# Performance work log

Hardware: AMD Instinct MI355X
Metric: run time of the kernel (lower is better)

The kernel has to match this reference:

```python
import jax, jax.numpy as jnp
import numpy as np

H, C = 5, 128          # heads, hidden_channels
NUM_GRAPHS = 500
N_NODES, N_EDGES = 20000, 320000


def gat_layer(x, edge_attr, src, dst, W, We, a_src, a_dst, a_edge, b):
    """PyG GATConv with edge_dim, add_self_loops=True, fill_value='mean', concat heads."""
    N = x.shape[0]
    ed = edge_attr.dtype
    # self-loop edge_attr = scatter-mean of incoming edge_attr per target node
    deg = jax.ops.segment_sum(jnp.ones((dst.shape[0],), ed), dst, num_segments=N)
    loop_attr = jax.ops.segment_sum(edge_attr, dst, num_segments=N) / jnp.maximum(deg, 1.0)[:, None]
    loop = jnp.arange(N, dtype=src.dtype)
    s = jnp.concatenate([src, loop])
    d = jnp.concatenate([dst, loop])
    ea = jnp.concatenate([edge_attr, loop_attr], axis=0)
    h = (x @ W).reshape(N, H, C)            # [N,H,C]
    e = (ea @ We).reshape(-1, H, C)         # [E2,H,C]
    a_l = (h * a_src).sum(-1)               # [N,H]
    a_r = (h * a_dst).sum(-1)               # [N,H]
    a_e = (e * a_edge).sum(-1)              # [E2,H]
    alpha = jax.nn.leaky_relu(a_l[s] + a_r[d] + a_e, 0.2)
    # segment softmax over destination neighborhoods
    amax = jax.ops.segment_max(alpha, d, num_segments=N)
    ex = jnp.exp(alpha - amax[d])
    denom = jax.ops.segment_sum(ex, d, num_segments=N)
    att = ex / (denom[d] + 1e-16)           # [E2,H]
    msg = h[s] * att[..., None]             # [E2,H,C]
    out = jax.ops.segment_sum(msg, d, num_segments=N).reshape(N, H * C)
    return out + b


def setup_inputs() -> dict:
    key = jax.random.key(0)
    ks = jax.random.split(key, 24)
    p = lambda k, sh: (jax.random.normal(k, sh, dtype=jnp.float32) * 0.05)
    inp = {
        "x": jax.random.normal(ks[0], (N_NODES, 43), dtype=jnp.float32),
        "edge_attr": jax.random.normal(ks[1], (N_EDGES, 10), dtype=jnp.float32),
        "W1": p(ks[2], (43, H * C)),   "We1": p(ks[3], (10, H * C)),
        "asrc1": p(ks[4], (H, C)), "adst1": p(ks[5], (H, C)), "aedge1": p(ks[6], (H, C)),
        "b1": jnp.zeros((H * C,), jnp.float32),
        "W2": p(ks[7], (H * C, H * C)), "We2": p(ks[8], (10, H * C)),
        "asrc2": p(ks[9], (H, C)), "adst2": p(ks[10], (H, C)), "aedge2": p(ks[11], (H, C)),
        "b2": jnp.zeros((H * C,), jnp.float32),
        "W3": p(ks[12], (H * C, H * C)), "We3": p(ks[13], (10, H * C)),
        "asrc3": p(ks[14], (H, C)), "adst3": p(ks[15], (H, C)), "aedge3": p(ks[16], (H, C)),
        "b3": jnp.zeros((H * C,), jnp.float32),
        "Wlin": p(ks[17], (H * C, 1)), "blin": jnp.zeros((1,), jnp.float32),
        "edge_index": jax.random.randint(ks[18], (2, N_EDGES), 0, N_NODES, dtype=jnp.int32),
        "batch": jnp.sort(jax.random.randint(ks[19], (N_NODES,), 0, NUM_GRAPHS, dtype=jnp.int32)),
    }
    return inp


def reference(x, edge_attr, W1, We1, asrc1, adst1, aedge1, b1,
              W2, We2, asrc2, adst2, aedge2, b2,
              W3, We3, asrc3, adst3, aedge3, b3,
              Wlin, blin, edge_index, batch):
    src, dst = edge_index[0], edge_index[1]
    h = jax.nn.relu(gat_layer(x, edge_attr, src, dst, W1, We1, asrc1, adst1, aedge1, b1))
    h = jax.nn.relu(gat_layer(h, edge_attr, src, dst, W2, We2, asrc2, adst2, aedge2, b2))
    h = gat_layer(h, edge_attr, src, dst, W3, We3, asrc3, adst3, aedge3, b3)
    # global mean pool over graphs
    cnt = jax.ops.segment_sum(jnp.ones((h.shape[0],), h.dtype), batch, num_segments=NUM_GRAPHS)
    pooled = jax.ops.segment_sum(h, batch, num_segments=NUM_GRAPHS) / jnp.maximum(cnt, 1.0)[:, None]
    return (pooled @ Wlin + blin).squeeze(-1)   # [NUM_GRAPHS]
```

## Files before the change

kernel.cpp:

```cpp
#include <hip/hip_runtime.h>

#define N_NODESC 20000
#define N_EDGESC 320000
#define HC 640
#define NGRAPH 500

typedef unsigned short u16;
typedef unsigned int u32;
typedef __attribute__((ext_vector_type(8))) short bf16x8;
typedef __attribute__((ext_vector_type(4))) float f32x4;

__device__ __forceinline__ float wred_sum(float v){
  #pragma unroll
  for(int o=32;o;o>>=1) v += __shfl_xor(v,o,64);
  return v;
}
__device__ __forceinline__ float lrelu(float x){ return x>0.f? x:0.2f*x; }

__device__ __forceinline__ u16 f2bf(float f){
  u32 u=__float_as_uint(f);
  u32 r=u+0x7FFFu+((u>>16)&1u);
  return (u16)(r>>16);
}
__device__ __forceinline__ float bf2f(u16 s){ return __uint_as_float(((u32)s)<<16); }
__device__ __forceinline__ float bflo(u32 w){ return __uint_as_float(w<<16); }
__device__ __forceinline__ float bfhi(u32 w){ return __uint_as_float(w&0xFFFF0000u); }

__device__ __forceinline__ void gload16(const void* g, void* l){
  __builtin_amdgcn_global_load_lds((const __attribute__((address_space(1))) void*)g,
                                   (__attribute__((address_space(3))) void*)l, 16, 0, 0);
}


__global__ void k_count(const int* __restrict__ dst, int* __restrict__ cnt){
  int i=blockIdx.x*blockDim.x+threadIdx.x;
  if(i>=N_EDGESC) return;
  atomicAdd(&cnt[dst[i]],1);
}

__global__ void k_scan(const int* __restrict__ cnt, int* __restrict__ rptr, int* __restrict__ pos){
  __shared__ int ps[1024];
  int t=threadIdx.x;
  const int CH=20;
  int beg=t*CH, end=min(beg+CH, N_NODESC);
  int s=0;
  for(int i=beg;i<end;i++) s+=cnt[i];
  ps[t]=s; __syncthreads();
  for(int off=1;off<1024;off<<=1){
    int v=(t>=off)? ps[t-off]:0;
    __syncthreads();
    ps[t]+=v;
    __syncthreads();
  }
  int base=ps[t]-s;
  for(int i=beg;i<end;i++){ rptr[i]=base; pos[i]=base; base+=cnt[i]; }
}

__global__ void k_scatter(const int* __restrict__ dst, int* __restrict__ pos,
                          int* __restrict__ eidx, int* __restrict__ dstC){
  int i=blockIdx.x*blockDim.x+threadIdx.x;
  if(i>=N_EDGESC) return;
  int d=dst[i];
  int j=atomicAdd(&pos[d],1);
  eidx[j]=i;
  dstC[j]=d;
}

__global__ void k_csr_edges(const int* __restrict__ eidx, const int* __restrict__ src,
                            const float* __restrict__ eattr,
                            int* __restrict__ srcE, float* __restrict__ eattrC){
  int j=blockIdx.x*blockDim.x+threadIdx.x;
  if(j>=N_EDGESC) return;
  int e=eidx[j];
  srcE[j]=src[e];
  const float* ep=&eattr[(size_t)e*10];
  float* op=&eattrC[(size_t)j*10];
  #pragma unroll
  for(int k=0;k<10;k++) op[k]=ep[k];
}

__global__ __launch_bounds__(256) void k_loop_attr(const float* __restrict__ eattrC,
    const int* __restrict__ rptr, const int* __restrict__ cnt,
    float* __restrict__ lattr){
  int tid=threadIdx.x, lane=tid&63;
  int n=blockIdx.x*4+(tid>>6);
  if(n>=N_NODESC) return;
  int beg=rptr[n], deg=cnt[n];
  float s[10]={0,0,0,0,0,0,0,0,0,0};
  for(int off=lane; off<deg; off+=64){
    const float* ep=&eattrC[(size_t)(beg+off)*10];
    #pragma unroll
    for(int k=0;k<10;k++) s[k]+=ep[k];
  }
  float inv=1.f/fmaxf((float)deg,1.f);
  #pragma unroll
  for(int k=0;k<10;k++){
    float tot=wred_sum(s[k]);
    if(lane==0) lattr[(size_t)n*10+k]=tot*inv;
  }
}


__global__ void k_conv_x(const float* __restrict__ x, u16* __restrict__ hi, u16* __restrict__ lo){
  int idx=blockIdx.x*blockDim.x+threadIdx.x;
  if(idx>=N_NODESC*64) return;
  int n=idx>>6, kk=idx&63;
  float v = kk<43 ? x[n*43+kk] : 0.f;
  u16 h=f2bf(v);
  hi[idx]=h; lo[idx]=f2bf(v-bf2f(h));
}

__global__ void k_conv_w3(const float* __restrict__ W0, const float* __restrict__ W1,
                          const float* __restrict__ W2,
                          u16* __restrict__ hi, u16* __restrict__ lo){
  const int R0=HC*64, R1=R0+HC*HC;
  const int TOT=R1+HC*HC;
  int idx=blockIdx.x*blockDim.x+threadIdx.x;
  if(idx>=TOT) return;
  const float* W; int local, KP, KL, base;
  if(idx<R0){ W=W0; local=idx; KP=64; KL=43; base=0; }
  else if(idx<R1){ W=W1; local=idx-R0; KP=HC; KL=HC; base=R0; }
  else { W=W2; local=idx-R1; KP=HC; KL=HC; base=R1; }
  int n=local/KP, kk=local-n*KP;
  float v = kk<KL ? W[(size_t)kk*HC+n] : 0.f;
  u16 h=f2bf(v);
  hi[base+local]=h;
  lo[base+local]=f2bf(v-bf2f(h));
}


__global__ void k_ve3(const float* __restrict__ We0, const float* __restrict__ ae0,
                      const float* __restrict__ We1, const float* __restrict__ ae1,
                      const float* __restrict__ We2, const float* __restrict__ ae2,
                      float* __restrict__ ve3){
  int t=threadIdx.x;
  if(t>=150) return;
  int L=t/50, r=t-50*L, k=r/5, h=r%5;
  const float* We = (L==0)?We0:(L==1)?We1:We2;
  const float* ae = (L==0)?ae0:(L==1)?ae1:ae2;
  float s=0.f;
  for(int c=0;c<128;c++) s += We[k*HC + h*128 + c]*ae[h*128+c];
  ve3[t]=s;
}

__global__ void k_cb(const float* __restrict__ bias, const float* __restrict__ wlin,
                     float* __restrict__ cb){
  int lane=threadIdx.x;
  float s=0.f;
  for(int c=lane;c<HC;c+=64) s+=bias[c]*wlin[c];
  s=wred_sum(s);
  if(lane==0) cb[0]=s;
}

__global__ __launch_bounds__(256) void k_edge_terms3(const float* __restrict__ eattrC,
    const float* __restrict__ lattr, const float* __restrict__ ve3,
    float* __restrict__ aeC3, float* __restrict__ ael3){
  __shared__ float ves[150];
  if(threadIdx.x<150) ves[threadIdx.x]=ve3[threadIdx.x];
  __syncthreads();
  const int NEDGET=N_EDGESC+N_NODESC*5;
  int idx=blockIdx.x*blockDim.x+threadIdx.x;
  if(idx>=3*NEDGET) return;
  int L=idx/NEDGET, r=idx-L*NEDGET;
  const float* vl=&ves[L*50];
  if(r<N_EDGESC){
    float ev[10];
    const float* ep=&eattrC[(size_t)r*10];
    #pragma unroll
    for(int k=0;k<10;k++) ev[k]=ep[k];
    #pragma unroll
    for(int hh=0;hh<5;hh++){
      float s=0.f;
      #pragma unroll
      for(int k=0;k<10;k++) s+=ev[k]*vl[k*5+hh];
      aeC3[(size_t)L*N_EDGESC*5 + (size_t)r*5+hh]=s;
    }
  }else{
    int t=r-N_EDGESC;
    int n=t/5, h=t-5*n;
    float s=0.f;
    #pragma unroll
    for(int k=0;k<10;k++) s+=lattr[(size_t)n*10+k]*vl[k*5+h];
    ael3[(size_t)L*N_NODESC*5 + t]=s;
  }
}

__global__ void k_edgew(const int* __restrict__ srcE, const int* __restrict__ dstC,
                        const float* __restrict__ al, const float* __restrict__ ar,
                        const float* __restrict__ aeC, float* __restrict__ wE){
  int j=blockIdx.x*blockDim.x+threadIdx.x;
  if(j>=N_EDGESC) return;
  int s=srcE[j], d=dstC[j];
  const float* av=&aeC[(size_t)j*5];
  float* wp=&wE[(size_t)j*5];
  #pragma unroll
  for(int h=0;h<5;h++)
    wp[h]=__expf(lrelu(al[s*5+h]+ar[d*5+h]+av[h]));
}


__global__ __launch_bounds__(256,3) void k_gemm_l0(
    const u16* __restrict__ Ahi, const u16* __restrict__ Alo,
    const u16* __restrict__ Bhi, const u16* __restrict__ Blo,
    const float* __restrict__ asrc, const float* __restrict__ adst,
    u16* __restrict__ hb, float* __restrict__ al, float* __restrict__ ar,
    int M, int KP, int nblk){
  constexpr int TERMS=4;
  constexpr int BOFF =8192;
  __shared__ u16 lds[2*TERMS*4096];
  int tid=threadIdx.x;
  int lane=tid&63;
  int w=tid>>6;
  int l15=lane&15, lg=lane>>4;
  int orig=blockIdx.x;
  int q=nblk>>3, r=nblk&7;
  int xcd=orig&7, off=orig>>3;
  int wg=(xcd<r? xcd*(q+1) : r*(q+1)+(xcd-r)*q)+off;
  int by=wg/5, bx=wg-5*by;
  int row0=by*128, col0=bx*128;
  int wr=w>>1, wc=w&1;

  f32x4 zero = {0.f,0.f,0.f,0.f};
  f32x4 acc[4][4];
  #pragma unroll
  for(int i=0;i<4;i++)
    #pragma unroll
    for(int j=0;j<4;j++) acc[i][j]=zero;

  auto stage=[&](int b, int k0){
    u16* base = lds + b*TERMS*4096;
    #pragma unroll
    for(int c=0;c<2;c++){
      int sb=w+4*c;
      int col=k0+lg*8;
      size_t aoff=(size_t)(row0+sb*16+l15)*KP + col;
      size_t boff=(size_t)(col0+sb*16+l15)*KP + col;
      gload16(Ahi+aoff, base + sb*512);
      gload16(Alo+aoff, base+4096 + sb*512);
      gload16(Bhi+boff, base+BOFF + sb*512);
      gload16(Blo+boff, base+BOFF+4096 + sb*512);
    }
  };

  int nt=KP/32;
  stage(0,0);
  __syncthreads();
  int cur=0;
  for(int t=0;t<nt;t++){
    if(t+1<nt) stage(cur^1,(t+1)*32);
    u16* cb = lds + cur*TERMS*4096;
    bf16x8 ah[4], bh[4], alv[4], bl[4];
    #pragma unroll
    for(int i=0;i<4;i++){
      ah[i]=*(const bf16x8*)&cb[(wr*4+i)*512 + lane*8];
      bh[i]=*(const bf16x8*)&cb[BOFF+(wc*4+i)*512 + lane*8];
      alv[i]=*(const bf16x8*)&cb[4096+(wr*4+i)*512+lane*8];
      bl[i] =*(const bf16x8*)&cb[BOFF+4096+(wc*4+i)*512+lane*8];
    }
    #pragma unroll
    for(int i=0;i<4;i++)
      #pragma unroll
      for(int j=0;j<4;j++){
        acc[i][j]=__builtin_amdgcn_mfma_f32_16x16x32_bf16(ah[i], bh[j],acc[i][j],0,0,0);
        acc[i][j]=__builtin_amdgcn_mfma_f32_16x16x32_bf16(alv[i],bh[j],acc[i][j],0,0,0);
        acc[i][j]=__builtin_amdgcn_mfma_f32_16x16x32_bf16(ah[i], bl[j],acc[i][j],0,0,0);
      }
    __syncthreads();
    cur^=1;
  }

  float asv[4], adv[4];
  #pragma unroll
  for(int j=0;j<4;j++){
    int c=col0+wc*64+j*16+l15;
    asv[j]=asrc[c]; adv[j]=adst[c];
  }
  #pragma unroll
  for(int i=0;i<4;i++){
    #pragma unroll
    for(int j=0;j<4;j++){
      #pragma unroll
      for(int rr=0;rr<4;rr++){
        int row=row0+wr*64+i*16+lg*4+rr;
        if(row<M) hb[(size_t)row*HC + (j*16+l15)*10 + bx*2+wc]=f2bf(acc[i][j][rr]);
      }
    }
  }
  float* redAl=(float*)lds;
  float* redAr=redAl+256;
  #pragma unroll
  for(int i=0;i<4;i++){
    #pragma unroll
    for(int rr=0;rr<4;rr++){
      float sa=0.f, sd=0.f;
      #pragma unroll
      for(int j=0;j<4;j++){ sa+=acc[i][j][rr]*asv[j]; sd+=acc[i][j][rr]*adv[j]; }
      #pragma unroll
      for(int o=1;o<16;o<<=1){ sa+=__shfl_xor(sa,o,64); sd+=__shfl_xor(sd,o,64); }
      if(l15==0){
        int lr=wr*64+i*16+lg*4+rr;
        redAl[lr*2+wc]=sa; redAr[lr*2+wc]=sd;
      }
    }
  }
  __syncthreads();
  if(tid<128){
    int row=row0+tid;
    if(row<M){
      al[(size_t)row*5+bx]=redAl[tid*2]+redAl[tid*2+1];
      ar[(size_t)row*5+bx]=redAr[tid*2]+redAr[tid*2+1];
    }
  }
}

template<bool HB, bool QOUT>
__global__ __launch_bounds__(256,6) void k_gemm64(
    const u16* __restrict__ A,
    const u16* __restrict__ B,
    const float* __restrict__ asrc, const float* __restrict__ adst,
    const float* __restrict__ wlin,
    u16* __restrict__ hb, float* __restrict__ al, float* __restrict__ ar,
    float* __restrict__ qn,
    int M, int KP, int nblk){
  __shared__ u16 lds[2*6144];
  int tid=threadIdx.x;
  int lane=tid&63;
  int w=tid>>6;
  int l15=lane&15, lg=lane>>4;
  int orig=blockIdx.x;
  int q=nblk>>3, r=nblk&7;
  int xcd=orig&7, off=orig>>3;
  int wg=(xcd<r? xcd*(q+1) : r*(q+1)+(xcd-r)*q)+off;
  int by=wg/5, bx=wg-5*by;
  int row0=by*64, col0=bx*128;

  f32x4 zero = {0.f,0.f,0.f,0.f};
  f32x4 acc[4][2];
  #pragma unroll
  for(int i=0;i<4;i++){ acc[i][0]=zero; acc[i][1]=zero; }

  auto stage=[&](int b, int k0){
    u16* base = lds + b*6144;
    int colk=k0+lg*8;
    size_t aoff=(size_t)(row0+w*16+l15)*KP + colk;
    gload16(A+aoff, base + w*512);
    #pragma unroll
    for(int c=0;c<2;c++){
      int sb=w+4*c;
      size_t boff=(size_t)(col0+sb*16+l15)*KP + colk;
      gload16(B+boff, base+2048 + sb*512);
    }
  };

  int nt=KP/32;
  stage(0,0);
  __syncthreads();
  int cur=0;
  for(int t=0;t<nt;t++){
    if(t+1<nt) stage(cur^1,(t+1)*32);
    u16* cb = lds + cur*6144;
    bf16x8 ah[4], bh[2];
    #pragma unroll
    for(int i=0;i<4;i++) ah[i]=*(const bf16x8*)&cb[i*512 + lane*8];
    #pragma unroll
    for(int j=0;j<2;j++) bh[j]=*(const bf16x8*)&cb[2048+(w*2+j)*512 + lane*8];
    #pragma unroll
    for(int i=0;i<4;i++){
      acc[i][0]=__builtin_amdgcn_mfma_f32_16x16x32_bf16(ah[i],bh[0],acc[i][0],0,0,0);
      acc[i][1]=__builtin_amdgcn_mfma_f32_16x16x32_bf16(ah[i],bh[1],acc[i][1],0,0,0);
    }
    __syncthreads();
    cur^=1;
  }

  float asv[2], adv[2], wlv[2];
  #pragma unroll
  for(int j=0;j<2;j++){
    int c=col0+w*32+j*16+l15;
    asv[j]=asrc[c]; adv[j]=adst[c];
    if(QOUT) wlv[j]=wlin[c];
  }
  if(HB){
    #pragma unroll
    for(int i=0;i<4;i++){
      #pragma unroll
      for(int j=0;j<2;j++){
        #pragma unroll
        for(int rr=0;rr<4;rr++){
          int row=row0+i*16+lg*4+rr;
          if(row<M)
            hb[(size_t)row*HC + ((w&1)*32+j*16+l15)*10 + bx*2+(w>>1)]=f2bf(acc[i][j][rr]);
        }
      }
    }
  }
  float* redAl=(float*)lds;
  float* redAr=redAl+256;
  float* redQ =redAr+256;
  #pragma unroll
  for(int i=0;i<4;i++){
    #pragma unroll
    for(int rr=0;rr<4;rr++){
      float sa=0.f, sd=0.f, sq=0.f;
      #pragma unroll
      for(int j=0;j<2;j++){
        sa+=acc[i][j][rr]*asv[j];
        sd+=acc[i][j][rr]*adv[j];
        if(QOUT) sq+=acc[i][j][rr]*wlv[j];
      }
      #pragma unroll
      for(int o=1;o<16;o<<=1){
        sa+=__shfl_xor(sa,o,64); sd+=__shfl_xor(sd,o,64);
        if(QOUT) sq+=__shfl_xor(sq,o,64);
      }
      if(l15==0){
        int lr=i*16+lg*4+rr;
        redAl[lr*4+w]=sa; redAr[lr*4+w]=sd;
        if(QOUT) redQ[lr*4+w]=sq;
      }
    }
  }
  __syncthreads();
  if(tid<64){
    int row=row0+tid;
    if(row<M){
      al[(size_t)row*5+bx]=redAl[tid*4]+redAl[tid*4+1]+redAl[tid*4+2]+redAl[tid*4+3];
      ar[(size_t)row*5+bx]=redAr[tid*4]+redAr[tid*4+1]+redAr[tid*4+2]+redAr[tid*4+3];
      if(QOUT) qn[(size_t)row*5+bx]=redQ[tid*4]+redQ[tid*4+1]+redQ[tid*4+2]+redQ[tid*4+3];
    }
  }
}

__global__ __launch_bounds__(256) void k_agg(const u16* __restrict__ hb, const int* __restrict__ srcE,
    const int* __restrict__ rptr, const int* __restrict__ cnt,
    const float* __restrict__ al, const float* __restrict__ ar, const float* __restrict__ ael,
    const float* __restrict__ wE, const float* __restrict__ bias,
    u16* __restrict__ ohi){
  int tid=threadIdx.x, lane=tid&63;
  int n=blockIdx.x*4+(tid>>6);
  if(n>=N_NODESC) return;
  float den[5], acc[10];
  #pragma unroll
  for(int h=0;h<5;h++)
    den[h]=__expf(lrelu(al[n*5+h]+ar[n*5+h]+ael[n*5+h]));
  {
    const u32* sp=(const u32*)(hb+(size_t)n*HC+lane*10);
    #pragma unroll
    for(int j2=0;j2<5;j2++){
      u32 wv=sp[j2];
      acc[2*j2]  =den[j2]*bflo(wv);
      acc[2*j2+1]=den[j2]*bfhi(wv);
    }
  }
  int beg=rptr[n], end=beg+cnt[n];
  int j=beg;
  for(; j+3<end; j+=4){
    int sj[4];
    #pragma unroll
    for(int u=0;u<4;u++) sj[u]=srcE[j+u];
    float w[4][5];
    #pragma unroll
    for(int u=0;u<4;u++){
      const float* wp=&wE[(size_t)(j+u)*5];
      #pragma unroll
      for(int h=0;h<5;h++) w[u][h]=wp[h];
    }
    u32 wv[4][5];
    #pragma unroll
    for(int u=0;u<4;u++){
      const u32* hr=(const u32*)(hb+(size_t)sj[u]*HC+lane*10);
      #pragma unroll
      for(int j2=0;j2<5;j2++) wv[u][j2]=hr[j2];
    }
    #pragma unroll
    for(int u=0;u<4;u++){
      #pragma unroll
      for(int j2=0;j2<5;j2++){
        den[j2]+=w[u][j2];
        acc[2*j2]  +=w[u][j2]*bflo(wv[u][j2]);
        acc[2*j2+1]+=w[u][j2]*bfhi(wv[u][j2]);
      }
    }
  }
  for(; j<end; j++){
    int sj=srcE[j];
    const float* wp=&wE[(size_t)j*5];
    float w[5];
    #pragma unroll
    for(int h=0;h<5;h++){ w[h]=wp[h]; den[h]+=w[h]; }
    const u32* hr=(const u32*)(hb+(size_t)sj*HC+lane*10);
    #pragma unroll
    for(int j2=0;j2<5;j2++){
      u32 wv=hr[j2];
      acc[2*j2]  +=w[j2]*bflo(wv);
      acc[2*j2+1]+=w[j2]*bfhi(wv);
    }
  }
  #pragma unroll
  for(int k=0;k<10;k++){
    int ccol=lane+64*k;
    float vv=acc[k]/(den[k>>1]+1e-16f)+bias[ccol];
    vv=fmaxf(vv,0.f);
    ohi[(size_t)n*HC+ccol]=f2bf(vv);
  }
}

__global__ __launch_bounds__(256) void k_agg_last(const float* __restrict__ qn,
    const int* __restrict__ srcE, const int* __restrict__ rptr, const int* __restrict__ cnt,
    const float* __restrict__ al, const float* __restrict__ ar, const float* __restrict__ ael,
    const float* __restrict__ aeC, const float* __restrict__ cb,
    float* __restrict__ pnode){
  int tid=threadIdx.x;
  int sub=tid&15;
  int n=blockIdx.x*16+(tid>>4);
  if(n>=N_NODESC) return;
  float arn[5], den[5], qs[5];
  #pragma unroll
  for(int h=0;h<5;h++) arn[h]=ar[n*5+h];
  #pragma unroll
  for(int h=0;h<5;h++){ den[h]=0.f; qs[h]=0.f; }
  if(sub==0){
    #pragma unroll
    for(int h=0;h<5;h++){
      float pp=__expf(lrelu(al[n*5+h]+arn[h]+ael[n*5+h]));
      den[h]=pp; qs[h]=pp*qn[(size_t)n*5+h];
    }
  }
  int beg=rptr[n], deg=cnt[n];
  for(int off=sub; off<deg; off+=16){
    int j=beg+off;
    int s=srcE[j];
    const float* av=&aeC[(size_t)j*5];
    const float* qv=&qn[(size_t)s*5];
    #pragma unroll
    for(int h=0;h<5;h++){
      float pp=__expf(lrelu(al[s*5+h]+arn[h]+av[h]));
      den[h]+=pp; qs[h]+=pp*qv[h];
    }
  }
  #pragma unroll
  for(int h=0;h<5;h++){
    #pragma unroll
    for(int o=1;o<16;o<<=1){
      den[h]+=__shfl_xor(den[h],o,16);
      qs[h]+=__shfl_xor(qs[h],o,16);
    }
  }
  if(sub==0){
    float s=0.f;
    #pragma unroll
    for(int h=0;h<5;h++) s+=qs[h]/(den[h]+1e-16f);
    pnode[n]=s+cb[0];
  }
}

__global__ __launch_bounds__(256) void k_graphout(const float* __restrict__ pnode,
    const int* __restrict__ batch, const float* __restrict__ blin,
    float* __restrict__ out){
  int tid=threadIdx.x, lane=tid&63;
  int g=blockIdx.x*4+(tid>>6);
  if(g>=NGRAPH) return;
  auto lb=[&](int val){
    int lo=0, hi=N_NODESC;
    while(lo<hi){ int mid=(lo+hi)>>1; if(batch[mid]<val) lo=mid+1; else hi=mid; }
    return lo;
  };
  int s0=lb(g), s1=lb(g+1);
  float s=0.f;
  for(int i=s0+lane;i<s1;i+=64) s+=pnode[i];
  s=wred_sum(s);
  if(lane==0) out[g]=s/fmaxf((float)(s1-s0),1.f)+blin[0];
}


extern "C" void kernel_launch(void* const* d_in, const int* in_sizes, int n_in,
                              void* d_out, int out_size, void* d_ws, size_t ws_size,
                              hipStream_t stream){
  const float* x     = (const float*)d_in[0];
  const float* eattr = (const float*)d_in[1];
  const float* W[3]    ={(const float*)d_in[2],(const float*)d_in[8],(const float*)d_in[14]};
  const float* We[3]   ={(const float*)d_in[3],(const float*)d_in[9],(const float*)d_in[15]};
  const float* asrc[3] ={(const float*)d_in[4],(const float*)d_in[10],(const float*)d_in[16]};
  const float* adst[3] ={(const float*)d_in[5],(const float*)d_in[11],(const float*)d_in[17]};
  const float* aedge[3]={(const float*)d_in[6],(const float*)d_in[12],(const float*)d_in[18]};
  const float* bias[3] ={(const float*)d_in[7],(const float*)d_in[13],(const float*)d_in[19]};
  const float* Wlin  = (const float*)d_in[20];
  const float* blin  = (const float*)d_in[21];
  const int* eind    = (const int*)d_in[22];
  const int* srcp    = eind;
  const int* dstp    = eind + N_EDGESC;
  const int* batch   = (const int*)d_in[23];
  float* out = (float*)d_out;

  char* ws=(char*)d_ws;
  size_t o=0;
  auto alloc=[&](size_t bytes)->void*{ void* p=ws+o; o=(o+bytes+255)&~(size_t)255; return p; };
  u16* hb   =(u16*)alloc((size_t)N_NODESC*HC*2);
  u16* Ahi =(u16*)alloc((size_t)N_NODESC*HC*2);
  u16* Axhi=(u16*)alloc((size_t)N_NODESC*64*2);
  u16* Axlo=(u16*)alloc((size_t)N_NODESC*64*2);
  const int WB0=0, WB1=HC*64, WB2=WB1+HC*HC;
  u16* Bthi3=(u16*)alloc((size_t)(WB2+HC*HC)*2);
  u16* Btlo3=(u16*)alloc((size_t)(WB2+HC*HC)*2);
  float* al   =(float*)alloc((size_t)N_NODESC*5*4);
  float* ar   =(float*)alloc((size_t)N_NODESC*5*4);
  float* qn   =(float*)alloc((size_t)N_NODESC*5*4);
  float* ael3 =(float*)alloc((size_t)3*N_NODESC*5*4);
  float* aeC3 =(float*)alloc((size_t)3*N_EDGESC*5*4);
  float* wE   =(float*)alloc((size_t)N_EDGESC*5*4);
  float* lattr=(float*)alloc((size_t)N_NODESC*10*4);
  float* eattrC=(float*)alloc((size_t)N_EDGESC*10*4);
  float* ve3  =(float*)alloc(256*4);
  float* cbv  =(float*)alloc(64*4);
  float* pnode=(float*)alloc((size_t)N_NODESC*4);
  int* cntI   =(int*)alloc((size_t)N_NODESC*4);
  int* rptr   =(int*)alloc((size_t)N_NODESC*4);
  int* pos    =(int*)alloc((size_t)N_NODESC*4);
  int* eidx   =(int*)alloc((size_t)N_EDGESC*4);
  int* srcE   =(int*)alloc((size_t)N_EDGESC*4);
  int* dstC   =(int*)alloc((size_t)N_EDGESC*4);

  hipMemsetAsync(cntI,0,(size_t)N_NODESC*4,stream);

  k_count<<<(N_EDGESC+255)/256,256,0,stream>>>(dstp,cntI);
  k_scan<<<1,1024,0,stream>>>(cntI,rptr,pos);
  k_scatter<<<(N_EDGESC+255)/256,256,0,stream>>>(dstp,pos,eidx,dstC);
  k_csr_edges<<<(N_EDGESC+255)/256,256,0,stream>>>(eidx,srcp,eattr,srcE,eattrC);
  k_loop_attr<<<(N_NODESC+3)/4,256,0,stream>>>(eattrC,rptr,cntI,lattr);
  k_conv_x<<<(N_NODESC*64+255)/256,256,0,stream>>>(x,Axhi,Axlo);
  k_ve3<<<1,256,0,stream>>>(We[0],aedge[0],We[1],aedge[1],We[2],aedge[2],ve3);
  k_cb<<<1,64,0,stream>>>(bias[2],Wlin,cbv);
  {
    int tot=WB2+HC*HC;
    k_conv_w3<<<(tot+255)/256,256,0,stream>>>(W[0],W[1],W[2],Bthi3,Btlo3);
  }
  {
    const int NEDGET=N_EDGESC+N_NODESC*5;
    k_edge_terms3<<<(3*NEDGET+255)/256,256,0,stream>>>(eattrC,lattr,ve3,aeC3,ael3);
  }

  const int NBLK0=5*((N_NODESC+127)/128);
  const int NBLK64=5*((N_NODESC+63)/64);
  for(int L=0;L<3;L++){
    const float* aeL = aeC3 + (size_t)L*N_EDGESC*5;
    const float* aelL= ael3 + (size_t)L*N_NODESC*5;
    if(L==0){
      k_gemm_l0<<<NBLK0,256,0,stream>>>(Axhi,Axlo,Bthi3+WB0,Btlo3+WB0,
          asrc[L],adst[L],hb,al,ar,N_NODESC,64,NBLK0);
      k_edgew<<<(N_EDGESC+255)/256,256,0,stream>>>(srcE,dstC,al,ar,aeL,wE);
      k_agg<<<(N_NODESC+3)/4,256,0,stream>>>(hb,srcE,rptr,cntI,al,ar,aelL,wE,bias[L],Ahi);
    }else if(L==1){
      k_gemm64<true,false><<<NBLK64,256,0,stream>>>(Ahi,Bthi3+WB1,
          asrc[L],adst[L],Wlin,hb,al,ar,qn,N_NODESC,HC,NBLK64);
      k_edgew<<<(N_EDGESC+255)/256,256,0,stream>>>(srcE,dstC,al,ar,aeL,wE);
      k_agg<<<(N_NODESC+3)/4,256,0,stream>>>(hb,srcE,rptr,cntI,al,ar,aelL,wE,bias[L],Ahi);
    }else{
      k_gemm64<false,true><<<NBLK64,256,0,stream>>>(Ahi,Bthi3+WB2,
          asrc[L],adst[L],Wlin,hb,al,ar,qn,N_NODESC,HC,NBLK64);
      k_agg_last<<<(N_NODESC+15)/16,256,0,stream>>>(qn,srcE,rptr,cntI,al,ar,aelL,aeL,cbv,pnode);
    }
  }
  k_graphout<<<(NGRAPH+3)/4,256,0,stream>>>(pnode,batch,blin,out);
}
```

Before: 446.1 us.

## Store GEMM operands in MFMA fragment-tiled layout for contiguous LDS staging loads

```diff
diff --git a/kernel.cpp b/kernel.cpp
--- a/kernel.cpp
+++ b/kernel.cpp
@@ -29,6 +29,10 @@
 __device__ __forceinline__ void gload16(const void* g, void* l){
   __builtin_amdgcn_global_load_lds((const __attribute__((address_space(1))) void*)g,
                                    (__attribute__((address_space(3))) void*)l, 16, 0, 0);
+}
+
+__device__ __forceinline__ size_t fidx(int r, int k, int KB){
+  return ((size_t)(r>>4)*KB + (k>>5))*512 + (((k>>3)&3)*16 + (r&15))*8 + (k&7);
 }
 
 
@@ -107,7 +111,8 @@
   int n=idx>>6, kk=idx&63;
   float v = kk<43 ? x[n*43+kk] : 0.f;
   u16 h=f2bf(v);
-  hi[idx]=h; lo[idx]=f2bf(v-bf2f(h));
+  size_t off=fidx(n,kk,2);
+  hi[off]=h; lo[off]=f2bf(v-bf2f(h));
 }
 
 __global__ void k_conv_w3(const float* __restrict__ W0, const float* __restrict__ W1,
@@ -124,8 +129,9 @@
   int n=local/KP, kk=local-n*KP;
   float v = kk<KL ? W[(size_t)kk*HC+n] : 0.f;
   u16 h=f2bf(v);
-  hi[base+local]=h;
-  lo[base+local]=f2bf(v-bf2f(h));
+  size_t off=(size_t)base + fidx(n,kk,KP>>5);
+  hi[off]=h;
+  lo[off]=f2bf(v-bf2f(h));
 }
 
 
@@ -229,16 +235,16 @@
 
   auto stage=[&](int b, int k0){
     u16* base = lds + b*TERMS*4096;
+    int kb=k0>>5;
     #pragma unroll
     for(int c=0;c<2;c++){
       int sb=w+4*c;
-      int col=k0+lg*8;
-      size_t aoff=(size_t)(row0+sb*16+l15)*KP + col;
-      size_t boff=(size_t)(col0+sb*16+l15)*KP + col;
-      gload16(Ahi+aoff, base + sb*512);
-      gload16(Alo+aoff, base+4096 + sb*512);
-      gload16(Bhi+boff, base+BOFF + sb*512);
-      gload16(Blo+boff, base+BOFF+4096 + sb*512);
+      size_t af=((size_t)((row0>>4)+sb)*2 + kb)*512 + lane*8;
+      size_t bf=((size_t)((col0>>4)+sb)*2 + kb)*512 + lane*8;
+      gload16(Ahi+af, base + sb*512);
+      gload16(Alo+af, base+4096 + sb*512);
+      gload16(Bhi+bf, base+BOFF + sb*512);
+      gload16(Blo+bf, base+BOFF+4096 + sb*512);
     }
   };
 
@@ -333,6 +339,7 @@
   int wg=(xcd<r? xcd*(q+1) : r*(q+1)+(xcd-r)*q)+off;
   int by=wg/5, bx=wg-5*by;
   int row0=by*64, col0=bx*128;
+  int KB=KP>>5;
 
   f32x4 zero = {0.f,0.f,0.f,0.f};
   f32x4 acc[4][2];
@@ -341,14 +348,14 @@
 
   auto stage=[&](int b, int k0){
     u16* base = lds + b*6144;
-    int colk=k0+lg*8;
-    size_t aoff=(size_t)(row0+w*16+l15)*KP + colk;
-    gload16(A+aoff, base + w*512);
+    int kb=k0>>5;
+    size_t af=((size_t)((row0>>4)+w)*KB + kb)*512 + lane*8;
+    gload16(A+af, base + w*512);
     #pragma unroll
     for(int c=0;c<2;c++){
       int sb=w+4*c;
-      size_t boff=(size_t)(col0+sb*16+l15)*KP + colk;
-      gload16(B+boff, base+2048 + sb*512);
+      size_t bf=((size_t)((col0>>4)+sb)*KB + kb)*512 + lane*8;
+      gload16(B+bf, base+2048 + sb*512);
     }
   };
 
@@ -501,7 +508,7 @@
     int ccol=lane+64*k;
     float vv=acc[k]/(den[k>>1]+1e-16f)+bias[ccol];
     vv=fmaxf(vv,0.f);
-    ohi[(size_t)n*HC+ccol]=f2bf(vv);
+    ohi[fidx(n,ccol,20)]=f2bf(vv);
   }
 }
 
```

New measurement: 411.4 us. -7.8%, faster.
